# Optimization experiments

Hardware: AMD Instinct MI355X
Metric: run time of the kernel (lower is better)

The kernel has to match this reference:

```python
import jax, jax.numpy as jnp
import numpy as np

BS, UE, RX, D = 4, 8, 128, 64
D_OUT = 64


def setup_inputs() -> dict:
    key = jax.random.key(0)
    ks = jax.random.split(key, 8)
    s1 = 1.0 / np.sqrt(5 * D)
    s2 = 1.0 / np.sqrt(D)
    return {
        "x": jax.random.normal(ks[0], (BS, UE, RX, D), dtype=jnp.float32),
        "W1": jax.random.uniform(ks[1], (D, 5 * D), jnp.float32, -s1, s1),
        "b1": jax.random.uniform(ks[2], (D,), jnp.float32, -s1, s1),
        "ln_g": jnp.ones((D,), jnp.float32),
        "ln_b": jnp.zeros((D,), jnp.float32),
        "bias": jnp.zeros((D,), jnp.float32),
        "W2": jax.random.uniform(ks[3], (D_OUT, D), jnp.float32, -s2, s2),
        "b2": jax.random.uniform(ks[4], (D_OUT,), jnp.float32, -s2, s2),
    }


def reference(x, W1, b1, ln_g, ln_b, bias, W2, b2):
    bs, ue, rx, d = x.shape
    # diagonal mask [rx, rx, 1] broadcast over feature dim
    diag = jnp.eye(rx, dtype=x.dtype)[:, :, None]
    m = jnp.mean(x, axis=2, keepdims=True)          # [bs, ue, 1, d]
    # Five pairwise feature maps, each [bs, ue, rx, rx, d]
    x1 = x[:, :, :, None, :] * diag                 # diag_embed(x)
    x2 = jnp.broadcast_to(x[:, :, :, None, :], (bs, ue, rx, rx, d))  # row copy
    x3 = jnp.broadcast_to(x[:, :, None, :, :], (bs, ue, rx, rx, d))  # col copy
    x4 = m[:, :, :, None, :] * diag                 # diag_embed(mean)
    x5 = jnp.broadcast_to(m[:, :, :, None, :], (bs, ue, rx, rx, d))  # mean bcast
    xAll = jnp.concatenate([x1, x2, x3, x4, x5], axis=-1)  # [bs, ue, rx, rx, 5d]
    # fc1
    h = jnp.einsum("buijf,df->buijd", xAll, W1) + b1
    # LayerNorm over last dim (eps = 1e-5, torch default)
    mu = jnp.mean(h, axis=-1, keepdims=True)
    var = jnp.mean(jnp.square(h - mu), axis=-1, keepdims=True)
    h = (h - mu) * jax.lax.rsqrt(var + 1e-5) * ln_g + ln_b
    y = jax.nn.relu(h)
    # diagonal-masked learned bias
    y = y + bias * diag
    # fc2
    out = jnp.einsum("buijd,od->buijo", y, W2) + b2
    return out
```

## Files before the change

kernel.cpp:

```cpp
#include <hip/hip_runtime.h>
#include <stdint.h>

#define RX 128
#define NBU 32

typedef __attribute__((ext_vector_type(8))) short short8;
typedef __attribute__((ext_vector_type(4))) float f32x4;

#define WS_R1 0
#define WS_R2 262144
#define WS_R3 524288
#define WS_R4 786432
#define WS_R5 788480

#define LDP 68

__device__ __forceinline__ uint32_t cvtpk(float a, float b) {
    uint32_t r;
    asm("v_cvt_pk_bf16_f32 %0, %1, %2" : "=v"(r) : "v"(a), "v"(b));
    return r;
}

union S8U4 { short8 s8; uint32_t u[4]; };

__device__ __forceinline__ short8 pack8(const float* __restrict__ y) {
    S8U4 t;
    t.u[0] = cvtpk(y[0], y[1]);
    t.u[1] = cvtpk(y[2], y[3]);
    t.u[2] = cvtpk(y[4], y[5]);
    t.u[3] = cvtpk(y[6], y[7]);
    return t.s8;
}

__device__ __forceinline__ void ld16f(const float* __restrict__ p, int d0, int d1,
                                      float* __restrict__ o) {
    *(float4*)(o + 0)  = *(const float4*)(p + d0);
    *(float4*)(o + 4)  = *(const float4*)(p + d0 + 4);
    *(float4*)(o + 8)  = *(const float4*)(p + d1);
    *(float4*)(o + 12) = *(const float4*)(p + d1 + 4);
}

__global__ __launch_bounds__(192) void k_pre(const float* __restrict__ x,
                                             const float* __restrict__ W1,
                                             const float* __restrict__ b1,
                                             float* __restrict__ ws) {
    __shared__ float s[8256];
    const int t = threadIdx.x;
    const int blk = blockIdx.x;

    if (blk < 512) {
        const int r0 = blk * 8;
        if (t < 128)
            ((float4*)s)[t] = ((const float4*)(x + r0 * 64))[t];
        __syncthreads();
        const int arr = t >> 6;
        const int dp  = t & 63;
        const float* wrow = W1 + dp * 320 + arr * 64;
        float4 w[16];
#pragma unroll
        for (int fc = 0; fc < 16; ++fc) w[fc] = ((const float4*)wrow)[fc];
        float* dst = ws + (arr == 0 ? WS_R1 : arr == 1 ? WS_R2 : WS_R3);
#pragma unroll
        for (int r = 0; r < 8; ++r) {
            float acc = 0.f;
#pragma unroll
            for (int fc = 0; fc < 16; ++fc) {
                float4 xv = ((const float4*)(s + r * 64))[fc];
                acc = fmaf(xv.x, w[fc].x, acc);
                acc = fmaf(xv.y, w[fc].y, acc);
                acc = fmaf(xv.z, w[fc].z, acc);
                acc = fmaf(xv.w, w[fc].w, acc);
            }
            dst[(r0 + r) * 64 + dp] = acc;
        }
    } else {
        const int bu = blk - 512;
        const float* xb = x + bu * RX * 64;
        for (int idx = t; idx < 2048; idx += 192)
            ((float4*)s)[idx] = ((const float4*)xb)[idx];
        __syncthreads();
        if (t < 64) {
            float a0 = 0, a1 = 0, a2 = 0, a3 = 0;
            for (int r = 0; r < 128; r += 4) {
                a0 += s[(r + 0) * 64 + t];
                a1 += s[(r + 1) * 64 + t];
                a2 += s[(r + 2) * 64 + t];
                a3 += s[(r + 3) * 64 + t];
            }
            s[8192 + t] = (a0 + a1 + a2 + a3) * (1.0f / 128.0f);
        }
        __syncthreads();
        if (t < 128) {
            const int dp = t & 63, which = t >> 6;
            const float* wrow = W1 + dp * 320 + 192 + which * 64;
            float acc = which ? b1[dp] : 0.f;
#pragma unroll
            for (int fc = 0; fc < 16; ++fc) {
                float4 mv = ((const float4*)(s + 8192))[fc];
                float4 wv = ((const float4*)wrow)[fc];
                acc = fmaf(mv.x, wv.x, acc);
                acc = fmaf(mv.y, wv.y, acc);
                acc = fmaf(mv.z, wv.z, acc);
                acc = fmaf(mv.w, wv.w, acc);
            }
            (ws + (which ? WS_R5 : WS_R4))[bu * 64 + dp] = acc;
        }
    }
}

__global__ __launch_bounds__(256, 3) void k_main(const float* __restrict__ ws,
                                                 const float* __restrict__ ln_g,
                                                 const float* __restrict__ ln_b,
                                                 const float* __restrict__ bias,
                                                 const float* __restrict__ W2,
                                                 const float* __restrict__ b2,
                                                 float* __restrict__ out) {
    const float* R1  = ws + WS_R1;
    const float* R2  = ws + WS_R2;
    const float* R3  = ws + WS_R3;
    const float* r4  = ws + WS_R4;
    const float* r5b = ws + WS_R5;

    __shared__ float sR3[128 * LDP];

    const int t    = threadIdx.x;
    const int lane = t & 63;
    const int wid  = t >> 6;
    const int q    = lane >> 4;
    const int ml   = lane & 15;
    const int bu   = blockIdx.x >> 5;
    const int i0   = (blockIdx.x & 31) * 4;

    const int d0 = q * 8;
    const int d1 = 32 + q * 8;

    {
        const float* r3g = R3 + (size_t)bu * 8192;
#pragma unroll
        for (int c = 0; c < 8; ++c) {
            const int g = c * 256 + t;
            const int r = g >> 4, col = (g & 15) << 2;
            *(float4*)&sR3[r * LDP + col] = ((const float4*)r3g)[g];
        }
    }

    float gv[16], bbv[16];
    ld16f(ln_g, d0, d1, gv);
    ld16f(ln_b, d0, d1, bbv);

    short8 bf[4][2];
#pragma unroll
    for (int ot = 0; ot < 4; ++ot) {
#pragma unroll
        for (int kt = 0; kt < 2; ++kt) {
            const float* wp = W2 + (ot * 16 + ml) * 64 + kt * 32 + q * 8;
            float4 w0 = *(const float4*)wp;
            float4 w1 = *(const float4*)(wp + 4);
            S8U4 v;
            v.u[0] = cvtpk(w0.x, w0.y);
            v.u[1] = cvtpk(w0.z, w0.w);
            v.u[2] = cvtpk(w1.x, w1.y);
            v.u[3] = cvtpk(w1.z, w1.w);
            bf[ot][kt] = v.s8;
        }
    }
    f32x4 b2q[4];
#pragma unroll
    for (int ot = 0; ot < 4; ++ot)
        b2q[ot] = *(const f32x4*)(b2 + ot * 16 + q * 4);

    __syncthreads();

#pragma unroll
    for (int ip = 0; ip < 4; ++ip) {
        const int i   = i0 + ip;
        const int row = bu * 128 + i;
        const int it  = i >> 4, im = i & 15;

        float basev[16], tv[16];
        ld16f(R2 + (size_t)row * 64, d0, d1, basev);
        ld16f(r5b + bu * 64, d0, d1, tv);
#pragma unroll
        for (int s = 0; s < 16; ++s) basev[s] += tv[s];

        float* outB = out + (size_t)row * 8192;

#pragma unroll
        for (int p = 0; p < 2; ++p) {
            const int jt = p * 4 + wid;
            const int j  = jt * 16 + ml;

            float h[16];
            {
                const float* sp = sR3 + j * LDP;
                *(float4*)(h + 0)  = *(const float4*)(sp + d0);
                *(float4*)(h + 4)  = *(const float4*)(sp + d0 + 4);
                *(float4*)(h + 8)  = *(const float4*)(sp + d1);
                *(float4*)(h + 12) = *(const float4*)(sp + d1 + 4);
            }
#pragma unroll
            for (int s = 0; s < 16; ++s) h[s] += basev[s];

            const bool diag = (jt == it) && (ml == im);
            if (diag) {
                float da[16], db[16];
                ld16f(R1 + (size_t)row * 64, d0, d1, da);
                ld16f(r4 + bu * 64, d0, d1, db);
#pragma unroll
                for (int s = 0; s < 16; ++s) h[s] += da[s] + db[s];
            }

            float sum = 0.f, ss = 0.f;
#pragma unroll
            for (int s = 0; s < 16; ++s) { sum += h[s]; ss = fmaf(h[s], h[s], ss); }
            sum += __shfl_xor(sum, 16); sum += __shfl_xor(sum, 32);
            ss  += __shfl_xor(ss, 16);  ss  += __shfl_xor(ss, 32);
            const float mu  = sum * 0.015625f;
            const float var = ss * 0.015625f - mu * mu;
            const float inv = rsqrtf(var + 1e-5f);
            const float nmi = -mu * inv;

#pragma unroll
            for (int s = 0; s < 16; ++s) {
                float v = fmaf(fmaf(h[s], inv, nmi), gv[s], bbv[s]);
                h[s] = fmaxf(v, 0.f);
            }
            if (diag) {
                float bi[16];
                ld16f(bias, d0, d1, bi);
#pragma unroll
                for (int s = 0; s < 16; ++s) h[s] += bi[s];
            }

            const short8 a0 = pack8(h);
            const short8 a1 = pack8(h + 8);

            float* ob = outB + (size_t)j * 64 + q * 4;
#pragma unroll
            for (int ot = 0; ot < 4; ++ot) {
                f32x4 acc = b2q[ot];
                acc = __builtin_amdgcn_mfma_f32_16x16x32_bf16(bf[ot][0], a0, acc, 0, 0, 0);
                acc = __builtin_amdgcn_mfma_f32_16x16x32_bf16(bf[ot][1], a1, acc, 0, 0, 0);
                *(f32x4*)(ob + ot * 16) = acc;
            }
        }
    }
}

extern "C" void kernel_launch(void* const* d_in, const int* in_sizes, int n_in,
                              void* d_out, int out_size, void* d_ws, size_t ws_size,
                              hipStream_t stream) {
    const float* x    = (const float*)d_in[0];
    const float* W1   = (const float*)d_in[1];
    const float* b1   = (const float*)d_in[2];
    const float* ln_g = (const float*)d_in[3];
    const float* ln_b = (const float*)d_in[4];
    const float* bias = (const float*)d_in[5];
    const float* W2   = (const float*)d_in[6];
    const float* b2   = (const float*)d_in[7];
    float* ws  = (float*)d_ws;
    float* out = (float*)d_out;

    hipLaunchKernelGGL(k_pre, dim3(544), dim3(192), 0, stream, x, W1, b1, ws);
    hipLaunchKernelGGL(k_main, dim3(1024), dim3(256), 0, stream,
                       ws, ln_g, ln_b, bias, W2, b2, out);
}
```

Before: 176.1 us.

## Stage MFMA outputs through swizzled LDS for coalesced nontemporal stores; hold R3 in registers

Each wave now loads its R3 rows straight into registers instead of staging the whole block through shared memory behind a barrier. The MFMA output tiles are written to a per-wave, XOR-swizzled, double-buffered LDS region and read back so that each wave writes contiguous 1 KB chunks to global memory. Those writes use nontemporal stores. The goal is to replace the scattered 16-byte output stores with fully coalesced streaming writes on this store-bound kernel. The cost is extra LDS traffic and higher register pressure under a 3-waves-per-EU launch bound, and LDS reuse relies on wave-level ordering since there is no explicit barrier.

```diff
diff --git a/kernel.cpp b/kernel.cpp
--- a/kernel.cpp
+++ b/kernel.cpp
@@ -12,8 +12,6 @@
 #define WS_R3 524288
 #define WS_R4 786432
 #define WS_R5 788480
-
-#define LDP 68
 
 __device__ __forceinline__ uint32_t cvtpk(float a, float b) {
     uint32_t r;
@@ -121,7 +119,7 @@
     const float* r4  = ws + WS_R4;
     const float* r5b = ws + WS_R5;
 
-    __shared__ float sR3[128 * LDP];
+    __shared__ float sEpi[8192];
 
     const int t    = threadIdx.x;
     const int lane = t & 63;
@@ -134,14 +132,12 @@
     const int d0 = q * 8;
     const int d1 = 32 + q * 8;
 
-    {
-        const float* r3g = R3 + (size_t)bu * 8192;
-#pragma unroll
-        for (int c = 0; c < 8; ++c) {
-            const int g = c * 256 + t;
-            const int r = g >> 4, col = (g & 15) << 2;
-            *(float4*)&sR3[r * LDP + col] = ((const float4*)r3g)[g];
-        }
+    float r3f[2][16];
+#pragma unroll
+    for (int tt = 0; tt < 2; ++tt) {
+        const int jt = wid + tt * 4;
+        const float* rp = R3 + (size_t)bu * 8192 + (jt * 16 + ml) * 64;
+        ld16f(rp, d0, d1, r3f[tt]);
     }
 
     float gv[16], bbv[16];
@@ -169,8 +165,6 @@
     for (int ot = 0; ot < 4; ++ot)
         b2q[ot] = *(const f32x4*)(b2 + ot * 16 + q * 4);
 
-    __syncthreads();
-
 #pragma unroll
     for (int ip = 0; ip < 4; ++ip) {
         const int i   = i0 + ip;
@@ -183,23 +177,13 @@
 #pragma unroll
         for (int s = 0; s < 16; ++s) basev[s] += tv[s];
 
-        float* outB = out + (size_t)row * 8192;
-
 #pragma unroll
         for (int p = 0; p < 2; ++p) {
             const int jt = p * 4 + wid;
-            const int j  = jt * 16 + ml;
 
             float h[16];
-            {
-                const float* sp = sR3 + j * LDP;
-                *(float4*)(h + 0)  = *(const float4*)(sp + d0);
-                *(float4*)(h + 4)  = *(const float4*)(sp + d0 + 4);
-                *(float4*)(h + 8)  = *(const float4*)(sp + d1);
-                *(float4*)(h + 12) = *(const float4*)(sp + d1 + 4);
-            }
-#pragma unroll
-            for (int s = 0; s < 16; ++s) h[s] += basev[s];
+#pragma unroll
+            for (int s = 0; s < 16; ++s) h[s] = r3f[p][s] + basev[s];
 
             const bool diag = (jt == it) && (ml == im);
             if (diag) {
@@ -235,13 +219,23 @@
             const short8 a0 = pack8(h);
             const short8 a1 = pack8(h + 8);
 
-            float* ob = outB + (size_t)j * 64 + q * 4;
+            float* ep = sEpi + wid * 2048 + (((ip << 1) + p) & 1) * 1024;
 #pragma unroll
             for (int ot = 0; ot < 4; ++ot) {
                 f32x4 acc = b2q[ot];
                 acc = __builtin_amdgcn_mfma_f32_16x16x32_bf16(bf[ot][0], a0, acc, 0, 0, 0);
                 acc = __builtin_amdgcn_mfma_f32_16x16x32_bf16(bf[ot][1], a1, acc, 0, 0, 0);
-                *(f32x4*)(ob + ot * 16) = acc;
+                const int off = (ot * 16 + q * 4) ^ ((ml & 7) << 3);
+                *(f32x4*)(ep + ml * 64 + off) = acc;
+            }
+            float* gb = out + (size_t)row * 8192 + jt * 1024;
+#pragma unroll
+            for (int c = 0; c < 4; ++c) {
+                const int F  = c * 256 + lane * 4;
+                const int jl = F >> 6;
+                const int o  = F & 63;
+                f32x4 v = *(const f32x4*)(ep + jl * 64 + (o ^ ((jl & 7) << 3)));
+                __builtin_nontemporal_store(v, (f32x4*)(gb + F));
             }
         }
     }
```

Measured after the change: 208.0 us. +18.1%, slower.
